# Optimization experiments

Hardware: AMD Instinct MI355X
Metric: run time of the kernel (lower is better)

## Reference

```python
import jax, jax.numpy as jnp
import numpy as np

WS = 8          # window_size
SS = WS // 2    # shift_size

def window_partition(x, ws):
    B, H, W, C = x.shape
    x = x.reshape(B, H // ws, ws, W // ws, ws, C)
    return x.transpose(0, 1, 3, 2, 4, 5).reshape(-1, ws, ws, C)

def window_reverse(win, ws, H, W):
    B = win.shape[0] // ((H // ws) * (W // ws))
    x = win.reshape(B, H // ws, W // ws, ws, ws, -1)
    return x.transpose(0, 1, 3, 2, 4, 5).reshape(B, H, W, -1)

def rel_pos_index(ws):
    coords = np.stack(np.meshgrid(np.arange(ws), np.arange(ws), indexing='ij'))
    cf = coords.reshape(2, -1)
    rel = (cf[:, :, None] - cf[:, None, :]).transpose(1, 2, 0)
    rel[:, :, 0] += ws - 1
    rel[:, :, 1] += ws - 1
    rel[:, :, 0] *= 2 * ws - 1
    return rel.sum(-1)  # (ws*ws, ws*ws) int

def calc_mask(H, W, ws, ss):
    img = np.zeros((1, H, W, 1), np.float32)
    cnt = 0
    sl = (slice(0, -ws), slice(-ws, -ss), slice(-ss, None))
    for hs in sl:
        for wsl in sl:
            img[:, hs, wsl, :] = cnt
            cnt += 1
    mw = img.reshape(1, H // ws, ws, W // ws, ws, 1).transpose(0, 1, 3, 2, 4, 5).reshape(-1, ws * ws)
    diff = mw[:, None, :] - mw[:, :, None]
    return jnp.asarray(np.where(diff != 0, -100.0, 0.0).astype(np.float32))

def conv1x1(x, W):
    return jnp.einsum('bchw,oc->bohw', x, W)

def dwconv3(x, W):
    # depthwise 3x3, stride 1, pad 1; W: (C,1,3,3)
    return jax.lax.conv_general_dilated(x, W, (1, 1), 'SAME',
        dimension_numbers=('NCHW', 'OIHW', 'NCHW'), feature_group_count=W.shape[0])

def l2norm(x, axis):
    return x / jnp.maximum(jnp.linalg.norm(x, axis=axis, keepdims=True), 1e-12)

def _forward(x, Wq0, Wqdw0, Wkv0, Wkvdw0, Wq1, Wqdw1, Wkv1, Wkvdw1,
             Wproj0, Wproj1, temp0, temp1, rpb_table, Wds):
    b, c, h, w = x.shape
    heads = temp0.shape[0]
    ch = c // heads
    N = WS * WS
    idx = rel_pos_index(WS)
    rpb = rpb_table[idx.reshape(-1)].reshape(N, N, heads).transpose(2, 0, 1)  # (heads,N,N)
    h2, w2 = h // 2, w // 2
    # mask computed at half res, then repeat_interleave(1/0.5^2=4, dim=0)
    mask = jnp.repeat(calc_mask(h2, w2, WS, SS), 4, axis=0)  # (nW,N,N)

    # ---- pool level 0: global channel (transposed) attention at full res
    q = dwconv3(conv1x1(x, Wq0), Wqdw0)
    kv = dwconv3(conv1x1(x, Wkv0), Wkvdw0)
    q = l2norm(q.reshape(b, heads, ch, h * w), -1)
    k = l2norm(kv[:, :c].reshape(b, heads, ch, h * w), -1)
    v = kv[:, c:].reshape(b, heads, ch, h * w)
    attn = jax.nn.softmax(jnp.einsum('bhcn,bhdn->bhcd', q, k) * temp0, axis=-1)
    out0 = jnp.einsum('bhcd,bhdn->bhcn', attn, v)
    out0 = out0.transpose(0, 3, 1, 2).reshape(b, h * w, c) @ Wproj0.T
    out0 = out0.reshape(b, h, w, c).transpose(0, 3, 1, 2)

    # ---- pool level 1: shifted-window cosine attention, kv at half resolution
    xds = x.reshape(b, c, h2, 2, w2, 2).mean(axis=(3, 5))  # AvgPool2d(2,2)
    xds = xds + conv1x1(xds, Wds)                           # FPDownSamp
    qw = window_partition(x.transpose(0, 2, 3, 1), WS).reshape(-1, N, c) @ Wq1.T
    q = window_reverse(qw.reshape(-1, WS, WS, c), WS, h2, w2).transpose(0, 3, 1, 2)  # (4b,c,h2,w2)
    q = dwconv3(q, Wqdw1)
    kvw = window_partition(xds.transpose(0, 2, 3, 1), WS).reshape(-1, N, c) @ Wkv1.T
    kv = window_reverse(kvw.reshape(-1, WS, WS, 2 * c), WS, h2, w2).transpose(0, 3, 1, 2)  # (b,2c,h2,w2)
    kv = dwconv3(kv, Wkvdw1)
    q = jnp.roll(q, (-SS, -SS), axis=(-2, -1))
    kv = jnp.roll(kv, (-SS, -SS), axis=(-2, -1))
    kvp = window_partition(kv.transpose(0, 2, 3, 1), WS).transpose(0, 3, 1, 2)  # (nWk,2c,ws,ws)
    qp = window_partition(q.transpose(0, 2, 3, 1), WS).transpose(0, 3, 1, 2)    # (B_,c,ws,ws)
    B_ = qp.shape[0]
    q = l2norm(qp.reshape(B_, heads, ch, N), -2)
    k = l2norm(jnp.repeat(kvp[:, :c], 4, axis=0).reshape(B_, heads, ch, N), -2)
    v = jnp.repeat(kvp[:, c:], 4, axis=0).reshape(B_, heads, ch, N)
    attn = jnp.einsum('bhcn,bhcm->bhnm', q, k) * temp1 + rpb[None]
    nW = mask.shape[0]
    attn = (attn.reshape(B_ // nW, nW, heads, N, N) + mask[None, :, None]).reshape(B_, heads, N, N)
    attn = jax.nn.softmax(attn, axis=-1)
    out1 = jnp.einsum('bhnm,bhcm->bhnc', attn, v)  # (B_,heads,N,ch)
    out1 = out1.transpose(0, 2, 1, 3).reshape(B_, N, c) @ Wproj1.T
    out1 = window_reverse(out1.reshape(B_, WS, WS, c), WS, h, w)  # (b,h,w,c)
    out1 = jnp.roll(out1, (SS, SS), axis=(1, 2)).transpose(0, 3, 1, 2)
    return out0 + out1

def setup_inputs() -> dict:
    key = jax.random.key(0)
    ks = jax.random.split(key, 16)
    dim, heads = 192, 6
    b, h, w = 4, 256, 256
    s = 0.02
    def rn(k, shape):
        return jax.random.normal(k, shape, dtype=jnp.float32) * s
    return dict(
        x=jax.random.normal(ks[0], (b, dim, h, w), dtype=jnp.float32),
        Wq0=rn(ks[1], (dim, dim)),
        Wqdw0=rn(ks[2], (dim, 1, 3, 3)),
        Wkv0=rn(ks[3], (2 * dim, dim)),
        Wkvdw0=rn(ks[4], (2 * dim, 1, 3, 3)),
        Wq1=rn(ks[5], (dim, dim)),
        Wqdw1=rn(ks[6], (dim, 1, 3, 3)),
        Wkv1=rn(ks[7], (2 * dim, dim)),
        Wkvdw1=rn(ks[8], (2 * dim, 1, 3, 3)),
        Wproj0=rn(ks[9], (dim, dim)),
        Wproj1=rn(ks[10], (dim, dim)),
        temp0=jnp.ones((heads, 1, 1), jnp.float32),
        temp1=jnp.ones((heads, 1, 1), jnp.float32),
        rpb_table=rn(ks[11], ((2 * WS - 1) ** 2, heads)),
        Wds=rn(ks[12], (dim, dim)),
    )

def reference(x, Wq0, Wqdw0, Wkv0, Wkvdw0, Wq1, Wqdw1, Wkv1, Wkvdw1,
              Wproj0, Wproj1, temp0, temp1, rpb_table, Wds):
    return _forward(x, Wq0, Wqdw0, Wkv0, Wkvdw0, Wq1, Wqdw1, Wkv1, Wkvdw1,
                    Wproj0, Wproj1, temp0, temp1, rpb_table, Wds)
```

## Files before the change

### kernel.cpp

```cpp
#include <hip/hip_runtime.h>


template<int EPI, bool XT>
__global__ __launch_bounds__(256)
void gemm_k(const float* __restrict__ Wm, const float* __restrict__ X,
            float* __restrict__ Out, const float* __restrict__ G1,
            int K, int P, long wstride, long xstride, long ostride)
{
  const int b = blockIdx.z;
  const float* Wb = Wm + (long)b * wstride;
  const float* Xb = X  + (long)b * xstride;
  float*       Ob = Out + (long)b * ostride;
  const int p0 = blockIdx.x * 64, o0 = blockIdx.y * 64;

  __shared__ float Ws[16][68];
  __shared__ float Xs[16][68];
  const int tid = threadIdx.x;
  const int tx = tid & 15, ty = tid >> 4;
  float acc[4][4] = {};

  for (int k0 = 0; k0 < K; k0 += 16) {
    {
      const int c = tid & 15, r = tid >> 4;
      #pragma unroll
      for (int i = 0; i < 4; i++)
        Ws[c][r + 16*i] = Wb[(long)(o0 + r + 16*i) * K + k0 + c];
      if (!XT) {
        const int pp = tid & 63, rr = tid >> 6;
        #pragma unroll
        for (int i = 0; i < 4; i++)
          Xs[rr + 4*i][pp] = Xb[(long)(k0 + rr + 4*i) * P + p0 + pp];
      } else {
        const int cc = tid & 15, pr = tid >> 4;
        #pragma unroll
        for (int i = 0; i < 4; i++)
          Xs[cc][pr + 16*i] = Xb[(long)(p0 + pr + 16*i) * K + k0 + cc];
      }
    }
    __syncthreads();
    #pragma unroll
    for (int kk = 0; kk < 16; kk++) {
      const float4 a = *(const float4*)&Ws[kk][ty*4];
      const float4 v = *(const float4*)&Xs[kk][tx*4];
      acc[0][0] += a.x*v.x; acc[0][1] += a.x*v.y; acc[0][2] += a.x*v.z; acc[0][3] += a.x*v.w;
      acc[1][0] += a.y*v.x; acc[1][1] += a.y*v.y; acc[1][2] += a.y*v.z; acc[1][3] += a.y*v.w;
      acc[2][0] += a.z*v.x; acc[2][1] += a.z*v.y; acc[2][2] += a.z*v.z; acc[2][3] += a.z*v.w;
      acc[3][0] += a.w*v.x; acc[3][1] += a.w*v.y; acc[3][2] += a.w*v.z; acc[3][3] += a.w*v.w;
    }
    __syncthreads();
  }

  #pragma unroll
  for (int i = 0; i < 4; i++) {
    const int o = o0 + ty*4 + i;
    const long base = (long)o * P + p0 + tx*4;
    float4 r = make_float4(acc[i][0], acc[i][1], acc[i][2], acc[i][3]);
    if (EPI == 1) {
      const float4 xr = *(const float4*)&Xb[base];
      r.x += xr.x; r.y += xr.y; r.z += xr.z; r.w += xr.w;
    }
    if (EPI == 2) {
      float gv[4];
      #pragma unroll
      for (int j = 0; j < 4; j++) {
        const int p  = p0 + tx*4 + j;
        const int y  = p >> 8,        x  = p & 255;
        const int yy = (y + 252) & 255, xx = (x + 252) & 255;
        const int win = b*1024 + (yy>>3)*32 + (xx>>3);
        const int n   = ((yy&7)<<3) | (xx&7);
        gv[j] = G1[(long)o * 262144 + win*64 + n];
      }
      r.x += gv[0]; r.y += gv[1]; r.z += gv[2]; r.w += gv[3];
    }
    *(float4*)&Ob[base] = r;
  }
}

__global__ void dwconv_k(const float* __restrict__ in, const float* __restrict__ wd,
                         float* __restrict__ out, int Cc, int Hh, int Ww)
{
  const int y = blockIdx.x, bc = blockIdx.y;
  const int x = threadIdx.x;
  const int c = bc % Cc;
  const float* w9 = wd + c*9;
  const float* ip = in + (long)bc * Hh * Ww;
  float s = 0.f;
  #pragma unroll
  for (int dy = 0; dy < 3; dy++) {
    const int yy = y + dy - 1;
    if (yy < 0 || yy >= Hh) continue;
    const float* row = ip + (long)yy * Ww;
    #pragma unroll
    for (int dx = 0; dx < 3; dx++) {
      const int xx = x + dx - 1;
      if (xx >= 0 && xx < Ww) s += w9[dy*3+dx] * row[xx];
    }
  }
  out[(long)bc * Hh * Ww + (long)y * Ww + x] = s;
}

__global__ void dwshuf_k(const float* __restrict__ in, const float* __restrict__ wd,
                         float* __restrict__ out)
{
  const int y1 = blockIdx.x, bc = blockIdx.y;
  const int x1 = threadIdx.x;
  const int c = bc % 192, Bp = bc / 192;
  const int bq = Bp >> 2, q3 = Bp & 3;
  const float* w9 = wd + c*9;
  const float* ip = in + ((long)bq*192 + c) * 65536;
  float s = 0.f;
  #pragma unroll
  for (int dy = 0; dy < 3; dy++) {
    const int yy = y1 + dy - 1;
    if (yy < 0 || yy >= 128) continue;
    const int hi = yy >> 3, ry = yy & 7;
    const int wy = q3*8 + (hi >> 1);
    #pragma unroll
    for (int dx = 0; dx < 3; dx++) {
      const int xx = x1 + dx - 1;
      if (xx < 0 || xx >= 128) continue;
      const int wi = xx >> 3, rx = xx & 7;
      const int wx = ((hi & 1) << 4) + wi;
      s += w9[dy*3+dx] * ip[(wy*8 + ry)*256 + wx*8 + rx];
    }
  }
  out[(long)bc * 16384 + y1*128 + x1] = s;
}

__global__ void avgpool_k(const float* __restrict__ in, float* __restrict__ out)
{
  const int y = blockIdx.x, bc = blockIdx.y;
  const int x = threadIdx.x;
  const float* ip = in + (long)bc*65536 + (2*y)*256 + 2*x;
  out[(long)bc*16384 + y*128 + x] = 0.25f * (ip[0] + ip[1] + ip[256] + ip[257]);
}

__global__ __launch_bounds__(64)
void gram_k(const float* __restrict__ q, const float* __restrict__ k,
            float* __restrict__ G, float* __restrict__ nrm)
{
  const int chunk = blockIdx.x, h = blockIdx.y, b = blockIdx.z;
  const long base = ((long)b*192 + h*32) * 65536 + chunk*1024;
  __shared__ float Qs[64][36];
  __shared__ float Ks[64][36];
  const int tid = threadIdx.x;
  const int ty = tid >> 3, tx = tid & 7;
  const int cc = tid & 31;
  float acc[4][4] = {};
  float ssq = 0.f;

  for (int t = 0; t < 16; t++) {
    __syncthreads();
    #pragma unroll 8
    for (int c = 0; c < 32; c++) {
      Qs[tid][c] = q[base + (long)c*65536 + t*64 + tid];
      Ks[tid][c] = k[base + (long)c*65536 + t*64 + tid];
    }
    __syncthreads();
    {
      const float (*S)[36] = (tid < 32) ? Qs : Ks;
      float lo = 0.f;
      #pragma unroll 16
      for (int n = 0; n < 64; n++) { const float v = S[n][cc]; lo += v*v; }
      ssq += lo;
    }
    #pragma unroll 8
    for (int n = 0; n < 64; n++) {
      const float4 a = *(const float4*)&Qs[n][ty*4];
      const float4 v = *(const float4*)&Ks[n][tx*4];
      acc[0][0] += a.x*v.x; acc[0][1] += a.x*v.y; acc[0][2] += a.x*v.z; acc[0][3] += a.x*v.w;
      acc[1][0] += a.y*v.x; acc[1][1] += a.y*v.y; acc[1][2] += a.y*v.z; acc[1][3] += a.y*v.w;
      acc[2][0] += a.z*v.x; acc[2][1] += a.z*v.y; acc[2][2] += a.z*v.z; acc[2][3] += a.z*v.w;
      acc[3][0] += a.w*v.x; acc[3][1] += a.w*v.y; acc[3][2] += a.w*v.z; acc[3][3] += a.w*v.w;
    }
  }
  float* Gp = G + (long)(b*6 + h) * 1024;
  #pragma unroll
  for (int i = 0; i < 4; i++)
    #pragma unroll
    for (int j = 0; j < 4; j++)
      atomicAdd(&Gp[(ty*4 + i)*32 + tx*4 + j], acc[i][j]);
  atomicAdd(&nrm[(tid < 32 ? 0 : 768) + b*192 + h*32 + cc], ssq);
}

__global__ void softmax0_k(const float* __restrict__ G, const float* __restrict__ nrm,
                           const float* __restrict__ temp0, float* __restrict__ attn)
{
  const int bh = blockIdx.x;
  const int b = bh / 6, h = bh % 6;
  const int c = threadIdx.x;
  __shared__ float nks[32];
  nks[c] = fmaxf(sqrtf(nrm[768 + b*192 + h*32 + c]), 1e-12f);
  __syncthreads();
  const float nq = fmaxf(sqrtf(nrm[b*192 + h*32 + c]), 1e-12f);
  const float t = temp0[h];
  const float* g = G + (long)bh*1024 + c*32;
  float v[32];
  float mx = -1e30f;
  #pragma unroll
  for (int d = 0; d < 32; d++) { v[d] = g[d] / (nq * nks[d]) * t; mx = fmaxf(mx, v[d]); }
  float s = 0.f;
  #pragma unroll
  for (int d = 0; d < 32; d++) { v[d] = __expf(v[d] - mx); s += v[d]; }
  const float inv = 1.f / s;
  float* a = attn + (long)bh*1024 + c*32;
  #pragma unroll
  for (int d = 0; d < 32; d++) a[d] = v[d] * inv;
}

__global__ void m0_k(const float* __restrict__ Wp, const float* __restrict__ attn,
                     float* __restrict__ M0)
{
  const int o = blockIdx.x, b = blockIdx.y, m = threadIdx.x;
  const int h = m >> 5, d = m & 31;
  const float* a = attn + (long)(b*6 + h)*1024 + d;
  const float* w = Wp + (long)o*192 + h*32;
  float s = 0.f;
  #pragma unroll
  for (int c = 0; c < 32; c++) s += w[c] * a[c*32];
  M0[((long)b*192 + o)*192 + m] = s;
}

__global__ __launch_bounds__(256)
void wattn_k(const float* __restrict__ q1s, const float* __restrict__ kv1d,
             const float* __restrict__ rpb_table, const float* __restrict__ temp1,
             float* __restrict__ out1)
{
  const int kwin = blockIdx.x, head = blockIdx.y;
  const int tid = threadIdx.x;
  const int w = tid >> 6;
  const int lane = tid & 63;
  const int win = kwin*4 + w;

  const int qimg = win >> 8, hi = (win >> 4) & 15, wi = win & 15;
  const int kb = kwin >> 8, khi = (kwin >> 4) & 15, kwi = kwin & 15;
  const int mw  = kwin & 255;
  const int mhi = mw >> 4, mwi = mw & 15;

  __shared__ float Ks[32][64];
  __shared__ float Vs[32][64];
  __shared__ float nk[64];
  __shared__ int   cnt[64];
  __shared__ float rpbh[225];

  const int r  = lane >> 3, s_ = lane & 7;
  const int qy = (hi*8  + r + 4) & 127, qx = (wi*8  + s_ + 4) & 127;
  const int ky = (khi*8 + r + 4) & 127, kx = (kwi*8 + s_ + 4) & 127;

  const long qbase = ((long)qimg*192 + head*32) * 16384;
  const long kbase = ((long)kb*384  + head*32) * 16384;
  const long qoff = (long)qy*128 + qx;
  const long koff = (long)ky*128 + kx;

  #pragma unroll
  for (int i = 0; i < 8; i++) {
    const int ch = w*8 + i;
    Ks[ch][lane] = kv1d[kbase + (long)ch*16384 + koff];
    Vs[ch][lane] = kv1d[kbase + (long)(192 + ch)*16384 + koff];
  }
  if (w == 0) {
    const int gy = mhi*8 + r, gx = mwi*8 + s_;
    const int yid = (gy < 120) ? 0 : ((gy < 124) ? 1 : 2);
    const int xid = (gx < 120) ? 0 : ((gx < 124) ? 1 : 2);
    cnt[lane] = yid*3 + xid;
  }
  for (int i = tid; i < 225; i += 256) rpbh[i] = rpb_table[i*6 + head];

  float qreg[32];
  float nq = 0.f;
  #pragma unroll
  for (int ch = 0; ch < 32; ch++) {
    qreg[ch] = q1s[qbase + (long)ch*16384 + qoff];
    nq += qreg[ch]*qreg[ch];
  }
  nq = fmaxf(sqrtf(nq), 1e-12f);

  __syncthreads();

  if (w == 0) {
    float kk = 0.f;
    #pragma unroll
    for (int ch = 0; ch < 32; ch++) { const float v = Ks[ch][lane]; kk += v*v; }
    nk[lane] = fmaxf(sqrtf(kk), 1e-12f);
  }

  float sc[64];
  #pragma unroll
  for (int mg = 0; mg < 16; mg++) {
    float ax = 0.f, ay = 0.f, az = 0.f, aw = 0.f;
    #pragma unroll
    for (int ch = 0; ch < 32; ch++) {
      const float4 kv4 = *(const float4*)&Ks[ch][mg*4];
      const float qv = qreg[ch];
      ax += qv*kv4.x; ay += qv*kv4.y; az += qv*kv4.z; aw += qv*kv4.w;
    }
    sc[mg*4+0] = ax; sc[mg*4+1] = ay; sc[mg*4+2] = az; sc[mg*4+3] = aw;
  }

  __syncthreads();

  const float tmp = temp1[head];
  const float invnq = 1.f / nq;
  const int myc = cnt[lane];
  #pragma unroll
  for (int m = 0; m < 64; m++) {
    const int rm = m >> 3, sm = m & 7;
    const int idx = (r - rm + 7)*15 + (s_ - sm + 7);
    const float msk = (cnt[m] != myc) ? -100.f : 0.f;
    sc[m] = sc[m] * invnq / nk[m] * tmp + rpbh[idx] + msk;
  }

  float mx = sc[0];
  #pragma unroll
  for (int m = 1; m < 64; m++) mx = fmaxf(mx, sc[m]);
  float sum = 0.f;
  #pragma unroll
  for (int m = 0; m < 64; m++) { sc[m] = __expf(sc[m] - mx); sum += sc[m]; }
  const float inv = 1.f / sum;

  float acc[32];
  #pragma unroll
  for (int ch = 0; ch < 32; ch++) {
    float a = 0.f;
    #pragma unroll
    for (int mg = 0; mg < 16; mg++) {
      const float4 v4 = *(const float4*)&Vs[ch][mg*4];
      a += sc[mg*4+0]*v4.x + sc[mg*4+1]*v4.y + sc[mg*4+2]*v4.z + sc[mg*4+3]*v4.w;
    }
    acc[ch] = a * inv;
  }

  float* op = out1 + ((long)win*64 + lane)*192 + head*32;
  #pragma unroll
  for (int g = 0; g < 8; g++)
    *(float4*)&op[g*4] = make_float4(acc[g*4], acc[g*4+1], acc[g*4+2], acc[g*4+3]);
}

extern "C" void kernel_launch(void* const* d_in, const int* in_sizes, int n_in,
                              void* d_out, int out_size, void* d_ws, size_t ws_size,
                              hipStream_t stream)
{
  (void)in_sizes; (void)n_in; (void)out_size; (void)ws_size;
  const float* x      = (const float*)d_in[0];
  const float* Wq0    = (const float*)d_in[1];
  const float* Wqdw0  = (const float*)d_in[2];
  const float* Wkv0   = (const float*)d_in[3];
  const float* Wkvdw0 = (const float*)d_in[4];
  const float* Wq1    = (const float*)d_in[5];
  const float* Wqdw1  = (const float*)d_in[6];
  const float* Wkv1   = (const float*)d_in[7];
  const float* Wkvdw1 = (const float*)d_in[8];
  const float* Wproj0 = (const float*)d_in[9];
  const float* Wproj1 = (const float*)d_in[10];
  const float* temp0  = (const float*)d_in[11];
  const float* temp1  = (const float*)d_in[12];
  const float* rpbt   = (const float*)d_in[13];
  const float* Wds    = (const float*)d_in[14];

  char* ws = (char*)d_ws;
  const long UB = 201326592L;
  float* U1 = (float*)(ws);
  float* U2 = (float*)(ws + UB);
  float* U3 = (float*)(ws + 2*UB);
  char* tiny = ws + 3*UB;
  float* G     = (float*)(tiny);
  float* nrm   = (float*)(tiny + 98304);
  float* attn0 = (float*)(tiny + 104448);
  float* M0    = (float*)(tiny + 202752);

  float* S1   = U3;
  float* S2   = (float*)((char*)U3 + 50331648);
  float* S3   = U1;
  float* S4   = (float*)((char*)U1 + 100663296);
  float* q1lin = (float*)d_out;
  float* q1s  = U3;
  float* out1pre = (float*)d_out;
  float* out1w   = U1;

  const long XS  = 192L * 65536;
  const long XS2 = 192L * 16384;

  gemm_k<0,false><<<dim3(1024,3,4), 256, 0, stream>>>(Wq0, x, U1, nullptr, 192, 65536, 0L, XS, XS);
  dwconv_k<<<dim3(256,768), 256, 0, stream>>>(U1, Wqdw0, U2, 192, 256, 256);
  gemm_k<0,false><<<dim3(1024,3,4), 256, 0, stream>>>(Wkv0, x, U1, nullptr, 192, 65536, 0L, XS, XS);
  dwconv_k<<<dim3(256,768), 256, 0, stream>>>(U1, Wkvdw0, U3, 192, 256, 256);
  hipMemsetAsync(G, 0, 104448, stream);
  gram_k<<<dim3(64,6,4), 64, 0, stream>>>(U2, U3, G, nrm);
  softmax0_k<<<24, 32, 0, stream>>>(G, nrm, temp0, attn0);
  m0_k<<<dim3(192,4), 192, 0, stream>>>(Wproj0, attn0, M0);
  gemm_k<0,false><<<dim3(1024,3,4), 256, 0, stream>>>(Wkv0 + 192*192, x, U1, nullptr, 192, 65536, 0L, XS, XS);
  dwconv_k<<<dim3(256,768), 256, 0, stream>>>(U1, Wkvdw0 + 192*9, U2, 192, 256, 256);

  avgpool_k<<<dim3(128,768), 128, 0, stream>>>(x, S1);
  gemm_k<1,false><<<dim3(256,3,4), 256, 0, stream>>>(Wds, S1, S2, nullptr, 192, 16384, 0L, XS2, XS2);
  gemm_k<0,false><<<dim3(256,6,4), 256, 0, stream>>>(Wkv1, S2, S3, nullptr, 192, 16384, 0L, XS2, 384L*16384);
  dwconv_k<<<dim3(128,1536), 128, 0, stream>>>(S3, Wkvdw1, S4, 384, 128, 128);

  gemm_k<0,false><<<dim3(1024,3,4), 256, 0, stream>>>(Wq1, x, q1lin, nullptr, 192, 65536, 0L, XS, XS);
  dwshuf_k<<<dim3(128,3072), 128, 0, stream>>>(q1lin, Wqdw1, q1s);
  wattn_k<<<dim3(1024,6), 256, 0, stream>>>(q1s, S4, rpbt, temp1, out1pre);
  gemm_k<0,true><<<dim3(4096,3,1), 256, 0, stream>>>(Wproj1, out1pre, out1w, nullptr, 192, 262144, 0L, 0L, 0L);

  gemm_k<2,false><<<dim3(1024,3,4), 256, 0, stream>>>(M0, U2, (float*)d_out, out1w, 192, 65536, 36864L, XS, XS);
}
```

Baseline: 4.602 ms.

## Widen GEMM output tile to 192 rows and process two windows per thread in window attention

The GEMM now covers all 192 output channels in one block (12x4 accumulators per thread), so each X tile is loaded once instead of three times. The cost is more registers and fewer blocks in flight. The window attention kernel now uses 128 threads, and each thread handles two query windows that share the same K/V tile, which halves shared-memory staging per window. It also fuses the K-norm into the load loop and replaces the per-element mask comparison with a ballot bitmask that only runs for edge windows.

New measurement: 4.675 ms. Within noise of the previous version (+1.6%).

```diff
diff --git a/kernel.cpp b/kernel.cpp
--- a/kernel.cpp
+++ b/kernel.cpp
@@ -11,19 +11,19 @@
   const float* Wb = Wm + (long)b * wstride;
   const float* Xb = X  + (long)b * xstride;
   float*       Ob = Out + (long)b * ostride;
-  const int p0 = blockIdx.x * 64, o0 = blockIdx.y * 64;
-
-  __shared__ float Ws[16][68];
+  const int p0 = blockIdx.x * 64, o0 = blockIdx.y * 192;
+
+  __shared__ float Ws[16][204];
   __shared__ float Xs[16][68];
   const int tid = threadIdx.x;
   const int tx = tid & 15, ty = tid >> 4;
-  float acc[4][4] = {};
+  float acc[12][4] = {};
 
   for (int k0 = 0; k0 < K; k0 += 16) {
     {
       const int c = tid & 15, r = tid >> 4;
       #pragma unroll
-      for (int i = 0; i < 4; i++)
+      for (int i = 0; i < 12; i++)
         Ws[c][r + 16*i] = Wb[(long)(o0 + r + 16*i) * K + k0 + c];
       if (!XT) {
         const int pp = tid & 63, rr = tid >> 6;
@@ -40,19 +40,22 @@
     __syncthreads();
     #pragma unroll
     for (int kk = 0; kk < 16; kk++) {
-      const float4 a = *(const float4*)&Ws[kk][ty*4];
-      const float4 v = *(const float4*)&Xs[kk][tx*4];
-      acc[0][0] += a.x*v.x; acc[0][1] += a.x*v.y; acc[0][2] += a.x*v.z; acc[0][3] += a.x*v.w;
-      acc[1][0] += a.y*v.x; acc[1][1] += a.y*v.y; acc[1][2] += a.y*v.z; acc[1][3] += a.y*v.w;
-      acc[2][0] += a.z*v.x; acc[2][1] += a.z*v.y; acc[2][2] += a.z*v.z; acc[2][3] += a.z*v.w;
-      acc[3][0] += a.w*v.x; acc[3][1] += a.w*v.y; acc[3][2] += a.w*v.z; acc[3][3] += a.w*v.w;
+      const float4 xv = *(const float4*)&Xs[kk][tx*4];
+      #pragma unroll
+      for (int jq = 0; jq < 3; jq++) {
+        const float4 a = *(const float4*)&Ws[kk][ty*12 + jq*4];
+        acc[jq*4+0][0] += a.x*xv.x; acc[jq*4+0][1] += a.x*xv.y; acc[jq*4+0][2] += a.x*xv.z; acc[jq*4+0][3] += a.x*xv.w;
+        acc[jq*4+1][0] += a.y*xv.x; acc[jq*4+1][1] += a.y*xv.y; acc[jq*4+1][2] += a.y*xv.z; acc[jq*4+1][3] += a.y*xv.w;
+        acc[jq*4+2][0] += a.z*xv.x; acc[jq*4+2][1] += a.z*xv.y; acc[jq*4+2][2] += a.z*xv.z; acc[jq*4+2][3] += a.z*xv.w;
+        acc[jq*4+3][0] += a.w*xv.x; acc[jq*4+3][1] += a.w*xv.y; acc[jq*4+3][2] += a.w*xv.z; acc[jq*4+3][3] += a.w*xv.w;
+      }
     }
     __syncthreads();
   }
 
   #pragma unroll
-  for (int i = 0; i < 4; i++) {
-    const int o = o0 + ty*4 + i;
+  for (int i = 0; i < 12; i++) {
+    const int o = o0 + ty*12 + i;
     const long base = (long)o * P + p0 + tx*4;
     float4 r = make_float4(acc[i][0], acc[i][1], acc[i][2], acc[i][3]);
     if (EPI == 1) {
@@ -221,119 +224,160 @@
   M0[((long)b*192 + o)*192 + m] = s;
 }
 
-__global__ __launch_bounds__(256)
+__global__ __launch_bounds__(128)
 void wattn_k(const float* __restrict__ q1s, const float* __restrict__ kv1d,
              const float* __restrict__ rpb_table, const float* __restrict__ temp1,
              float* __restrict__ out1)
 {
   const int kwin = blockIdx.x, head = blockIdx.y;
   const int tid = threadIdx.x;
-  const int w = tid >> 6;
-  const int lane = tid & 63;
-  const int win = kwin*4 + w;
-
-  const int qimg = win >> 8, hi = (win >> 4) & 15, wi = win & 15;
+  const int w = tid >> 6, lane = tid & 63;
+  const int winA = kwin*4 + 2*w, winB = winA + 1;
+
+  const int qimg = winA >> 8;
+  const int hiA = (winA >> 4) & 15, wiA = winA & 15;
+  const int hiB = (winB >> 4) & 15, wiB = winB & 15;
   const int kb = kwin >> 8, khi = (kwin >> 4) & 15, kwi = kwin & 15;
-  const int mw  = kwin & 255;
-  const int mhi = mw >> 4, mwi = mw & 15;
+  const int mw  = kwin & 255, mhi = mw >> 4, mwi = mw & 15;
 
   __shared__ float Ks[32][64];
   __shared__ float Vs[32][64];
-  __shared__ float nk[64];
-  __shared__ int   cnt[64];
-  __shared__ float rpbh[225];
+  __shared__ float nkinv_s[64];
+  __shared__ float nkp[2][64];
+  __shared__ float rpbh[226];
 
   const int r  = lane >> 3, s_ = lane & 7;
-  const int qy = (hi*8  + r + 4) & 127, qx = (wi*8  + s_ + 4) & 127;
-  const int ky = (khi*8 + r + 4) & 127, kx = (kwi*8 + s_ + 4) & 127;
+  const int qyA = (hiA*8 + r + 4) & 127, qxA = (wiA*8 + s_ + 4) & 127;
+  const int qyB = (hiB*8 + r + 4) & 127, qxB = (wiB*8 + s_ + 4) & 127;
+  const int ky  = (khi*8 + r + 4) & 127, kx  = (kwi*8 + s_ + 4) & 127;
 
   const long qbase = ((long)qimg*192 + head*32) * 16384;
   const long kbase = ((long)kb*384  + head*32) * 16384;
-  const long qoff = (long)qy*128 + qx;
-  const long koff = (long)ky*128 + kx;
-
-  #pragma unroll
-  for (int i = 0; i < 8; i++) {
-    const int ch = w*8 + i;
-    Ks[ch][lane] = kv1d[kbase + (long)ch*16384 + koff];
-    Vs[ch][lane] = kv1d[kbase + (long)(192 + ch)*16384 + koff];
-  }
-  if (w == 0) {
+  const long qoffA = (long)qyA*128 + qxA;
+  const long qoffB = (long)qyB*128 + qxB;
+  const long koff  = (long)ky*128 + kx;
+
+  {
+    float kk = 0.f;
+    #pragma unroll
+    for (int i = 0; i < 16; i++) {
+      const int ch = w*16 + i;
+      const float kvl = kv1d[kbase + (long)ch*16384 + koff];
+      Ks[ch][lane] = kvl;
+      kk += kvl*kvl;
+      Vs[ch][lane] = kv1d[kbase + (long)(192 + ch)*16384 + koff];
+    }
+    nkp[w][lane] = kk;
+  }
+  for (int i = tid; i < 225; i += 128) rpbh[i] = rpb_table[i*6 + head];
+
+  const bool edge = (mhi == 15) || (mwi == 15);
+  unsigned long long bm = ~0ull;
+  if (edge) {
     const int gy = mhi*8 + r, gx = mwi*8 + s_;
     const int yid = (gy < 120) ? 0 : ((gy < 124) ? 1 : 2);
     const int xid = (gx < 120) ? 0 : ((gx < 124) ? 1 : 2);
-    cnt[lane] = yid*3 + xid;
-  }
-  for (int i = tid; i < 225; i += 256) rpbh[i] = rpb_table[i*6 + head];
-
-  float qreg[32];
-  float nq = 0.f;
-  #pragma unroll
-  for (int ch = 0; ch < 32; ch++) {
-    qreg[ch] = q1s[qbase + (long)ch*16384 + qoff];
-    nq += qreg[ch]*qreg[ch];
-  }
-  nq = fmaxf(sqrtf(nq), 1e-12f);
+    const int myc = yid*3 + xid;
+    #pragma unroll
+    for (int g = 0; g < 9; g++) {
+      const unsigned long long mgm = __ballot(myc == g);
+      if (myc == g) bm = mgm;
+    }
+  }
 
   __syncthreads();
 
-  if (w == 0) {
-    float kk = 0.f;
-    #pragma unroll
-    for (int ch = 0; ch < 32; ch++) { const float v = Ks[ch][lane]; kk += v*v; }
-    nk[lane] = fmaxf(sqrtf(kk), 1e-12f);
-  }
-
-  float sc[64];
-  #pragma unroll
-  for (int mg = 0; mg < 16; mg++) {
-    float ax = 0.f, ay = 0.f, az = 0.f, aw = 0.f;
-    #pragma unroll
-    for (int ch = 0; ch < 32; ch++) {
-      const float4 kv4 = *(const float4*)&Ks[ch][mg*4];
-      const float qv = qreg[ch];
-      ax += qv*kv4.x; ay += qv*kv4.y; az += qv*kv4.z; aw += qv*kv4.w;
-    }
-    sc[mg*4+0] = ax; sc[mg*4+1] = ay; sc[mg*4+2] = az; sc[mg*4+3] = aw;
+  if (tid < 64)
+    nkinv_s[lane] = 1.f / fmaxf(sqrtf(nkp[0][lane] + nkp[1][lane]), 1e-12f);
+
+  float scA[64], scB[64];
+  #pragma unroll
+  for (int m = 0; m < 64; m++) { scA[m] = 0.f; scB[m] = 0.f; }
+  float nqA = 0.f, nqB = 0.f;
+  #pragma unroll
+  for (int half = 0; half < 2; half++) {
+    float qA[16], qB[16];
+    #pragma unroll
+    for (int i = 0; i < 16; i++) {
+      const long co = (long)(half*16 + i)*16384;
+      qA[i] = q1s[qbase + co + qoffA];
+      qB[i] = q1s[qbase + co + qoffB];
+      nqA += qA[i]*qA[i];
+      nqB += qB[i]*qB[i];
+    }
+    #pragma unroll
+    for (int i = 0; i < 16; i++) {
+      const int ch = half*16 + i;
+      #pragma unroll
+      for (int mg = 0; mg < 16; mg++) {
+        const float4 k4 = *(const float4*)&Ks[ch][mg*4];
+        scA[mg*4+0] += qA[i]*k4.x; scA[mg*4+1] += qA[i]*k4.y;
+        scA[mg*4+2] += qA[i]*k4.z; scA[mg*4+3] += qA[i]*k4.w;
+        scB[mg*4+0] += qB[i]*k4.x; scB[mg*4+1] += qB[i]*k4.y;
+        scB[mg*4+2] += qB[i]*k4.z; scB[mg*4+3] += qB[i]*k4.w;
+      }
+    }
   }
 
   __syncthreads();
 
   const float tmp = temp1[head];
-  const float invnq = 1.f / nq;
-  const int myc = cnt[lane];
+  const float sA = tmp / fmaxf(sqrtf(nqA), 1e-12f);
+  const float sB = tmp / fmaxf(sqrtf(nqB), 1e-12f);
+  const int ib = (r + 7)*15 + (s_ + 7);
+  if (edge) {
+    #pragma unroll
+    for (int m = 0; m < 64; m++) {
+      const int rm = m >> 3, sm = m & 7;
+      float u = rpbh[ib - rm*15 - sm];
+      u += ((bm >> m) & 1ull) ? 0.f : -100.f;
+      const float t = nkinv_s[m];
+      scA[m] = scA[m]*t*sA + u;
+      scB[m] = scB[m]*t*sB + u;
+    }
+  } else {
+    #pragma unroll
+    for (int m = 0; m < 64; m++) {
+      const int rm = m >> 3, sm = m & 7;
+      const float u = rpbh[ib - rm*15 - sm];
+      const float t = nkinv_s[m];
+      scA[m] = scA[m]*t*sA + u;
+      scB[m] = scB[m]*t*sB + u;
+    }
+  }
+
+  float mxA = scA[0], mxB = scB[0];
+  #pragma unroll
+  for (int m = 1; m < 64; m++) { mxA = fmaxf(mxA, scA[m]); mxB = fmaxf(mxB, scB[m]); }
+  float suA = 0.f, suB = 0.f;
   #pragma unroll
   for (int m = 0; m < 64; m++) {
-    const int rm = m >> 3, sm = m & 7;
-    const int idx = (r - rm + 7)*15 + (s_ - sm + 7);
-    const float msk = (cnt[m] != myc) ? -100.f : 0.f;
-    sc[m] = sc[m] * invnq / nk[m] * tmp + rpbh[idx] + msk;
-  }
-
-  float mx = sc[0];
-  #pragma unroll
-  for (int m = 1; m < 64; m++) mx = fmaxf(mx, sc[m]);
-  float sum = 0.f;
-  #pragma unroll
-  for (int m = 0; m < 64; m++) { sc[m] = __expf(sc[m] - mx); sum += sc[m]; }
-  const float inv = 1.f / sum;
-
-  float acc[32];
-  #pragma unroll
-  for (int ch = 0; ch < 32; ch++) {
-    float a = 0.f;
-    #pragma unroll
-    for (int mg = 0; mg < 16; mg++) {
-      const float4 v4 = *(const float4*)&Vs[ch][mg*4];
-      a += sc[mg*4+0]*v4.x + sc[mg*4+1]*v4.y + sc[mg*4+2]*v4.z + sc[mg*4+3]*v4.w;
-    }
-    acc[ch] = a * inv;
-  }
-
-  float* op = out1 + ((long)win*64 + lane)*192 + head*32;
-  #pragma unroll
-  for (int g = 0; g < 8; g++)
-    *(float4*)&op[g*4] = make_float4(acc[g*4], acc[g*4+1], acc[g*4+2], acc[g*4+3]);
+    scA[m] = __expf(scA[m] - mxA); suA += scA[m];
+    scB[m] = __expf(scB[m] - mxB); suB += scB[m];
+  }
+  const float ivA = 1.f / suA, ivB = 1.f / suB;
+
+  float* opA = out1 + ((long)winA*64 + lane)*192 + head*32;
+  float* opB = out1 + ((long)winB*64 + lane)*192 + head*32;
+  #pragma unroll
+  for (int g = 0; g < 8; g++) {
+    float oA[4], oB[4];
+    #pragma unroll
+    for (int cc = 0; cc < 4; cc++) {
+      const int ch = g*4 + cc;
+      float aA = 0.f, aB = 0.f;
+      #pragma unroll
+      for (int mg = 0; mg < 16; mg++) {
+        const float4 v4 = *(const float4*)&Vs[ch][mg*4];
+        aA += scA[mg*4+0]*v4.x + scA[mg*4+1]*v4.y + scA[mg*4+2]*v4.z + scA[mg*4+3]*v4.w;
+        aB += scB[mg*4+0]*v4.x + scB[mg*4+1]*v4.y + scB[mg*4+2]*v4.z + scB[mg*4+3]*v4.w;
+      }
+      oA[cc] = aA * ivA;
+      oB[cc] = aB * ivB;
+    }
+    *(float4*)&opA[g*4] = make_float4(oA[0], oA[1], oA[2], oA[3]);
+    *(float4*)&opB[g*4] = make_float4(oB[0], oB[1], oB[2], oB[3]);
+  }
 }
 
 extern "C" void kernel_launch(void* const* d_in, const int* in_sizes, int n_in,
@@ -380,26 +424,26 @@
   const long XS  = 192L * 65536;
   const long XS2 = 192L * 16384;
 
-  gemm_k<0,false><<<dim3(1024,3,4), 256, 0, stream>>>(Wq0, x, U1, nullptr, 192, 65536, 0L, XS, XS);
+  gemm_k<0,false><<<dim3(1024,1,4), 256, 0, stream>>>(Wq0, x, U1, nullptr, 192, 65536, 0L, XS, XS);
   dwconv_k<<<dim3(256,768), 256, 0, stream>>>(U1, Wqdw0, U2, 192, 256, 256);
-  gemm_k<0,false><<<dim3(1024,3,4), 256, 0, stream>>>(Wkv0, x, U1, nullptr, 192, 65536, 0L, XS, XS);
+  gemm_k<0,false><<<dim3(1024,1,4), 256, 0, stream>>>(Wkv0, x, U1, nullptr, 192, 65536, 0L, XS, XS);
   dwconv_k<<<dim3(256,768), 256, 0, stream>>>(U1, Wkvdw0, U3, 192, 256, 256);
   hipMemsetAsync(G, 0, 104448, stream);
   gram_k<<<dim3(64,6,4), 64, 0, stream>>>(U2, U3, G, nrm);
   softmax0_k<<<24, 32, 0, stream>>>(G, nrm, temp0, attn0);
   m0_k<<<dim3(192,4), 192, 0, stream>>>(Wproj0, attn0, M0);
-  gemm_k<0,false><<<dim3(1024,3,4), 256, 0, stream>>>(Wkv0 + 192*192, x, U1, nullptr, 192, 65536, 0L, XS, XS);
+  gemm_k<0,false><<<dim3(1024,1,4), 256, 0, stream>>>(Wkv0 + 192*192, x, U1, nullptr, 192, 65536, 0L, XS, XS);
   dwconv_k<<<dim3(256,768), 256, 0, stream>>>(U1, Wkvdw0 + 192*9, U2, 192, 256, 256);
 
   avgpool_k<<<dim3(128,768), 128, 0, stream>>>(x, S1);
-  gemm_k<1,false><<<dim3(256,3,4), 256, 0, stream>>>(Wds, S1, S2, nullptr, 192, 16384, 0L, XS2, XS2);
-  gemm_k<0,false><<<dim3(256,6,4), 256, 0, stream>>>(Wkv1, S2, S3, nullptr, 192, 16384, 0L, XS2, 384L*16384);
+  gemm_k<1,false><<<dim3(256,1,4), 256, 0, stream>>>(Wds, S1, S2, nullptr, 192, 16384, 0L, XS2, XS2);
+  gemm_k<0,false><<<dim3(256,2,4), 256, 0, stream>>>(Wkv1, S2, S3, nullptr, 192, 16384, 0L, XS2, 384L*16384);
   dwconv_k<<<dim3(128,1536), 128, 0, stream>>>(S3, Wkvdw1, S4, 384, 128, 128);
 
-  gemm_k<0,false><<<dim3(1024,3,4), 256, 0, stream>>>(Wq1, x, q1lin, nullptr, 192, 65536, 0L, XS, XS);
+  gemm_k<0,false><<<dim3(1024,1,4), 256, 0, stream>>>(Wq1, x, q1lin, nullptr, 192, 65536, 0L, XS, XS);
   dwshuf_k<<<dim3(128,3072), 128, 0, stream>>>(q1lin, Wqdw1, q1s);
-  wattn_k<<<dim3(1024,6), 256, 0, stream>>>(q1s, S4, rpbt, temp1, out1pre);
-  gemm_k<0,true><<<dim3(4096,3,1), 256, 0, stream>>>(Wproj1, out1pre, out1w, nullptr, 192, 262144, 0L, 0L, 0L);
-
-  gemm_k<2,false><<<dim3(1024,3,4), 256, 0, stream>>>(M0, U2, (float*)d_out, out1w, 192, 65536, 36864L, XS, XS);
-}
+  wattn_k<<<dim3(1024,6), 128, 0, stream>>>(q1s, S4, rpbt, temp1, out1pre);
+  gemm_k<0,true><<<dim3(4096,1,1), 256, 0, stream>>>(Wproj1, out1pre, out1w, nullptr, 192, 262144, 0L, 0L, 0L);
+
+  gemm_k<2,false><<<dim3(1024,1,4), 256, 0, stream>>>(M0, U2, (float*)d_out, out1w, 192, 65536, 36864L, XS, XS);
+}
```

## Widen GEMM tile to all 192 outputs and streamline window attention scoring

Applied to the files above, without the earlier changes.

The GEMM kernel now computes 192 output channels per block, each thread holding 12x4 accumulators, so every input tile is loaded from global memory once instead of three times. All launches shrink their y-dimension to match. The window attention kernel folds the key-norm computation into the K load, replaces the shared count-array mask with a wavefront ballot bitmask that is only built for edge windows, and precomputes scale factors. This trades more registers per thread and lower occupancy for fewer redundant global reads and less per-score arithmetic.

Measured after the change: 4.124 ms. 1.12x faster.

```diff
diff --git a/kernel.cpp b/kernel.cpp
--- a/kernel.cpp
+++ b/kernel.cpp
@@ -11,19 +11,19 @@
   const float* Wb = Wm + (long)b * wstride;
   const float* Xb = X  + (long)b * xstride;
   float*       Ob = Out + (long)b * ostride;
-  const int p0 = blockIdx.x * 64, o0 = blockIdx.y * 64;
-
-  __shared__ float Ws[16][68];
+  const int p0 = blockIdx.x * 64, o0 = blockIdx.y * 192;
+
+  __shared__ float Ws[16][204];
   __shared__ float Xs[16][68];
   const int tid = threadIdx.x;
   const int tx = tid & 15, ty = tid >> 4;
-  float acc[4][4] = {};
+  float acc[12][4] = {};
 
   for (int k0 = 0; k0 < K; k0 += 16) {
     {
       const int c = tid & 15, r = tid >> 4;
       #pragma unroll
-      for (int i = 0; i < 4; i++)
+      for (int i = 0; i < 12; i++)
         Ws[c][r + 16*i] = Wb[(long)(o0 + r + 16*i) * K + k0 + c];
       if (!XT) {
         const int pp = tid & 63, rr = tid >> 6;
@@ -40,19 +40,22 @@
     __syncthreads();
     #pragma unroll
     for (int kk = 0; kk < 16; kk++) {
-      const float4 a = *(const float4*)&Ws[kk][ty*4];
-      const float4 v = *(const float4*)&Xs[kk][tx*4];
-      acc[0][0] += a.x*v.x; acc[0][1] += a.x*v.y; acc[0][2] += a.x*v.z; acc[0][3] += a.x*v.w;
-      acc[1][0] += a.y*v.x; acc[1][1] += a.y*v.y; acc[1][2] += a.y*v.z; acc[1][3] += a.y*v.w;
-      acc[2][0] += a.z*v.x; acc[2][1] += a.z*v.y; acc[2][2] += a.z*v.z; acc[2][3] += a.z*v.w;
-      acc[3][0] += a.w*v.x; acc[3][1] += a.w*v.y; acc[3][2] += a.w*v.z; acc[3][3] += a.w*v.w;
+      const float4 xv = *(const float4*)&Xs[kk][tx*4];
+      #pragma unroll
+      for (int jq = 0; jq < 3; jq++) {
+        const float4 a = *(const float4*)&Ws[kk][ty*12 + jq*4];
+        acc[jq*4+0][0] += a.x*xv.x; acc[jq*4+0][1] += a.x*xv.y; acc[jq*4+0][2] += a.x*xv.z; acc[jq*4+0][3] += a.x*xv.w;
+        acc[jq*4+1][0] += a.y*xv.x; acc[jq*4+1][1] += a.y*xv.y; acc[jq*4+1][2] += a.y*xv.z; acc[jq*4+1][3] += a.y*xv.w;
+        acc[jq*4+2][0] += a.z*xv.x; acc[jq*4+2][1] += a.z*xv.y; acc[jq*4+2][2] += a.z*xv.z; acc[jq*4+2][3] += a.z*xv.w;
+        acc[jq*4+3][0] += a.w*xv.x; acc[jq*4+3][1] += a.w*xv.y; acc[jq*4+3][2] += a.w*xv.z; acc[jq*4+3][3] += a.w*xv.w;
+      }
     }
     __syncthreads();
   }
 
   #pragma unroll
-  for (int i = 0; i < 4; i++) {
-    const int o = o0 + ty*4 + i;
+  for (int i = 0; i < 12; i++) {
+    const int o = o0 + ty*12 + i;
     const long base = (long)o * P + p0 + tx*4;
     float4 r = make_float4(acc[i][0], acc[i][1], acc[i][2], acc[i][3]);
     if (EPI == 1) {
@@ -228,20 +231,18 @@
 {
   const int kwin = blockIdx.x, head = blockIdx.y;
   const int tid = threadIdx.x;
-  const int w = tid >> 6;
-  const int lane = tid & 63;
+  const int w = tid >> 6, lane = tid & 63;
   const int win = kwin*4 + w;
 
   const int qimg = win >> 8, hi = (win >> 4) & 15, wi = win & 15;
   const int kb = kwin >> 8, khi = (kwin >> 4) & 15, kwi = kwin & 15;
-  const int mw  = kwin & 255;
-  const int mhi = mw >> 4, mwi = mw & 15;
+  const int mw  = kwin & 255, mhi = mw >> 4, mwi = mw & 15;
 
   __shared__ float Ks[32][64];
   __shared__ float Vs[32][64];
-  __shared__ float nk[64];
-  __shared__ int   cnt[64];
-  __shared__ float rpbh[225];
+  __shared__ float nkp[4][64];
+  __shared__ float nkinv_s[64];
+  __shared__ float rpbh[226];
 
   const int r  = lane >> 3, s_ = lane & 7;
   const int qy = (hi*8  + r + 4) & 127, qx = (wi*8  + s_ + 4) & 127;
@@ -252,37 +253,47 @@
   const long qoff = (long)qy*128 + qx;
   const long koff = (long)ky*128 + kx;
 
-  #pragma unroll
-  for (int i = 0; i < 8; i++) {
-    const int ch = w*8 + i;
-    Ks[ch][lane] = kv1d[kbase + (long)ch*16384 + koff];
-    Vs[ch][lane] = kv1d[kbase + (long)(192 + ch)*16384 + koff];
-  }
-  if (w == 0) {
+  {
+    float kk = 0.f;
+    #pragma unroll
+    for (int i = 0; i < 8; i++) {
+      const int ch = w*8 + i;
+      const float kvl = kv1d[kbase + (long)ch*16384 + koff];
+      Ks[ch][lane] = kvl;
+      kk += kvl*kvl;
+      Vs[ch][lane] = kv1d[kbase + (long)(192 + ch)*16384 + koff];
+    }
+    nkp[w][lane] = kk;
+  }
+  for (int i = tid; i < 225; i += 256) rpbh[i] = rpb_table[i*6 + head];
+
+  float qreg[32];
+  float nq = 0.f;
+  #pragma unroll
+  for (int ch = 0; ch < 32; ch++) {
+    qreg[ch] = q1s[qbase + (long)ch*16384 + qoff];
+    nq += qreg[ch]*qreg[ch];
+  }
+
+  const bool edge = (mhi == 15) || (mwi == 15);
+  unsigned long long bm = ~0ull;
+  if (edge) {
     const int gy = mhi*8 + r, gx = mwi*8 + s_;
     const int yid = (gy < 120) ? 0 : ((gy < 124) ? 1 : 2);
     const int xid = (gx < 120) ? 0 : ((gx < 124) ? 1 : 2);
-    cnt[lane] = yid*3 + xid;
-  }
-  for (int i = tid; i < 225; i += 256) rpbh[i] = rpb_table[i*6 + head];
-
-  float qreg[32];
-  float nq = 0.f;
-  #pragma unroll
-  for (int ch = 0; ch < 32; ch++) {
-    qreg[ch] = q1s[qbase + (long)ch*16384 + qoff];
-    nq += qreg[ch]*qreg[ch];
-  }
-  nq = fmaxf(sqrtf(nq), 1e-12f);
+    const int myc = yid*3 + xid;
+    #pragma unroll
+    for (int g = 0; g < 9; g++) {
+      const unsigned long long mgm = __ballot(myc == g);
+      if (myc == g) bm = mgm;
+    }
+  }
 
   __syncthreads();
 
-  if (w == 0) {
-    float kk = 0.f;
-    #pragma unroll
-    for (int ch = 0; ch < 32; ch++) { const float v = Ks[ch][lane]; kk += v*v; }
-    nk[lane] = fmaxf(sqrtf(kk), 1e-12f);
-  }
+  if (tid < 64)
+    nkinv_s[lane] = 1.f / fmaxf(sqrtf(nkp[0][lane] + nkp[1][lane] +
+                                      nkp[2][lane] + nkp[3][lane]), 1e-12f);
 
   float sc[64];
   #pragma unroll
@@ -290,24 +301,31 @@
     float ax = 0.f, ay = 0.f, az = 0.f, aw = 0.f;
     #pragma unroll
     for (int ch = 0; ch < 32; ch++) {
-      const float4 kv4 = *(const float4*)&Ks[ch][mg*4];
+      const float4 k4 = *(const float4*)&Ks[ch][mg*4];
       const float qv = qreg[ch];
-      ax += qv*kv4.x; ay += qv*kv4.y; az += qv*kv4.z; aw += qv*kv4.w;
+      ax += qv*k4.x; ay += qv*k4.y; az += qv*k4.z; aw += qv*k4.w;
     }
     sc[mg*4+0] = ax; sc[mg*4+1] = ay; sc[mg*4+2] = az; sc[mg*4+3] = aw;
   }
 
   __syncthreads();
 
-  const float tmp = temp1[head];
-  const float invnq = 1.f / nq;
-  const int myc = cnt[lane];
-  #pragma unroll
-  for (int m = 0; m < 64; m++) {
-    const int rm = m >> 3, sm = m & 7;
-    const int idx = (r - rm + 7)*15 + (s_ - sm + 7);
-    const float msk = (cnt[m] != myc) ? -100.f : 0.f;
-    sc[m] = sc[m] * invnq / nk[m] * tmp + rpbh[idx] + msk;
+  const float sA = temp1[head] / fmaxf(sqrtf(nq), 1e-12f);
+  const int ib = (r + 7)*15 + (s_ + 7);
+  if (edge) {
+    #pragma unroll
+    for (int m = 0; m < 64; m++) {
+      const int rm = m >> 3, sm = m & 7;
+      float u = rpbh[ib - rm*15 - sm];
+      u += ((bm >> m) & 1ull) ? 0.f : -100.f;
+      sc[m] = sc[m] * nkinv_s[m] * sA + u;
+    }
+  } else {
+    #pragma unroll
+    for (int m = 0; m < 64; m++) {
+      const int rm = m >> 3, sm = m & 7;
+      sc[m] = sc[m] * nkinv_s[m] * sA + rpbh[ib - rm*15 - sm];
+    }
   }
 
   float mx = sc[0];
@@ -380,26 +398,26 @@
   const long XS  = 192L * 65536;
   const long XS2 = 192L * 16384;
 
-  gemm_k<0,false><<<dim3(1024,3,4), 256, 0, stream>>>(Wq0, x, U1, nullptr, 192, 65536, 0L, XS, XS);
+  gemm_k<0,false><<<dim3(1024,1,4), 256, 0, stream>>>(Wq0, x, U1, nullptr, 192, 65536, 0L, XS, XS);
   dwconv_k<<<dim3(256,768), 256, 0, stream>>>(U1, Wqdw0, U2, 192, 256, 256);
-  gemm_k<0,false><<<dim3(1024,3,4), 256, 0, stream>>>(Wkv0, x, U1, nullptr, 192, 65536, 0L, XS, XS);
+  gemm_k<0,false><<<dim3(1024,1,4), 256, 0, stream>>>(Wkv0, x, U1, nullptr, 192, 65536, 0L, XS, XS);
   dwconv_k<<<dim3(256,768), 256, 0, stream>>>(U1, Wkvdw0, U3, 192, 256, 256);
   hipMemsetAsync(G, 0, 104448, stream);
   gram_k<<<dim3(64,6,4), 64, 0, stream>>>(U2, U3, G, nrm);
   softmax0_k<<<24, 32, 0, stream>>>(G, nrm, temp0, attn0);
   m0_k<<<dim3(192,4), 192, 0, stream>>>(Wproj0, attn0, M0);
-  gemm_k<0,false><<<dim3(1024,3,4), 256, 0, stream>>>(Wkv0 + 192*192, x, U1, nullptr, 192, 65536, 0L, XS, XS);
+  gemm_k<0,false><<<dim3(1024,1,4), 256, 0, stream>>>(Wkv0 + 192*192, x, U1, nullptr, 192, 65536, 0L, XS, XS);
   dwconv_k<<<dim3(256,768), 256, 0, stream>>>(U1, Wkvdw0 + 192*9, U2, 192, 256, 256);
 
   avgpool_k<<<dim3(128,768), 128, 0, stream>>>(x, S1);
-  gemm_k<1,false><<<dim3(256,3,4), 256, 0, stream>>>(Wds, S1, S2, nullptr, 192, 16384, 0L, XS2, XS2);
-  gemm_k<0,false><<<dim3(256,6,4), 256, 0, stream>>>(Wkv1, S2, S3, nullptr, 192, 16384, 0L, XS2, 384L*16384);
+  gemm_k<1,false><<<dim3(256,1,4), 256, 0, stream>>>(Wds, S1, S2, nullptr, 192, 16384, 0L, XS2, XS2);
+  gemm_k<0,false><<<dim3(256,2,4), 256, 0, stream>>>(Wkv1, S2, S3, nullptr, 192, 16384, 0L, XS2, 384L*16384);
   dwconv_k<<<dim3(128,1536), 128, 0, stream>>>(S3, Wkvdw1, S4, 384, 128, 128);
 
-  gemm_k<0,false><<<dim3(1024,3,4), 256, 0, stream>>>(Wq1, x, q1lin, nullptr, 192, 65536, 0L, XS, XS);
+  gemm_k<0,false><<<dim3(1024,1,4), 256, 0, stream>>>(Wq1, x, q1lin, nullptr, 192, 65536, 0L, XS, XS);
   dwshuf_k<<<dim3(128,3072), 128, 0, stream>>>(q1lin, Wqdw1, q1s);
   wattn_k<<<dim3(1024,6), 256, 0, stream>>>(q1s, S4, rpbt, temp1, out1pre);
-  gemm_k<0,true><<<dim3(4096,3,1), 256, 0, stream>>>(Wproj1, out1pre, out1w, nullptr, 192, 262144, 0L, 0L, 0L);
-
-  gemm_k<2,false><<<dim3(1024,3,4), 256, 0, stream>>>(M0, U2, (float*)d_out, out1w, 192, 65536, 36864L, XS, XS);
-}
+  gemm_k<0,true><<<dim3(4096,1,1), 256, 0, stream>>>(Wproj1, out1pre, out1w, nullptr, 192, 262144, 0L, 0L, 0L);
+
+  gemm_k<2,false><<<dim3(1024,1,4), 256, 0, stream>>>(M0, U2, (float*)d_out, out1w, 192, 65536, 36864L, XS, XS);
+}
```
